# Kernel tuning notes

Hardware: AMD Instinct MI355X
Metric: run time of the kernel (lower is better)

## Reference

```python
import jax, jax.numpy as jnp
import numpy as np

H = 12
DK = 64


def setup_inputs() -> dict:
    key = jax.random.key(0)
    ks = jax.random.split(key, 6)
    bs, ne, d = 32, 20, H * DK
    R = jax.random.normal(ks[0], (bs, ne, ne, d), dtype=jnp.float32)
    R_mas = jax.random.randint(ks[1], (bs, ne, ne, 1), 0, 2).astype(jnp.float32)
    WQ_w = jax.random.normal(ks[2], (DK, DK), dtype=jnp.float32) * (1.0 / np.sqrt(DK))
    WK_w = jax.random.normal(ks[3], (DK, DK), dtype=jnp.float32) * (1.0 / np.sqrt(DK))
    WV_w = jax.random.normal(ks[4], (DK, DK), dtype=jnp.float32) * (1.0 / np.sqrt(DK))
    zb = jnp.zeros((DK,), dtype=jnp.float32)
    return {"R": R, "R_mas": R_mas, "WQ_w": WQ_w, "WQ_b": zb, "WK_w": WK_w,
            "WK_b": zb, "WV_w": WV_w, "WV_b": zb}


def reference(R, R_mas, WQ_w, WQ_b, WK_w, WK_b, WV_w, WV_b):
    bs, ne, _, d = R.shape
    h, dk = H, DK
    n = ne * ne
    # (bs, h, ne, ne, dk)
    Rh = R.reshape(bs, ne, ne, h, dk).transpose(0, 3, 1, 2, 4)
    # per-head QKV linears (torch Linear: y = x @ W.T + b)
    Q = (Rh @ WQ_w.T + WQ_b).reshape(bs, h, n, dk)
    K = (Rh @ WK_w.T + WK_b).reshape(bs, h, n, dk)
    V = (Rh @ WV_w.T + WV_b).reshape(bs, h, n, dk)
    mas = R_mas.reshape(bs, 1, n)                      # (bs,1,n)
    att_mas = mas[:, :, :, None] * mas[:, :, None, :]  # (bs,1,n,n)
    alpha = jnp.einsum('bhqd,bhkd->bhqk', Q, K)        # (bs,h,n,n)
    alpha = alpha - (1.0 - att_mas) * 100000.0         # mask BEFORE scaling (faithful)
    alpha = jax.nn.softmax(alpha / jnp.sqrt(jnp.float32(dk)), axis=-1)
    R_Z = jnp.einsum('bhqk,bhkd->bhqd', alpha, V).reshape(bs, h, ne, ne, dk)
    R_Z = R_Z * R_mas.reshape(bs, 1, ne, ne, 1)
    # (bs, ne, ne, h*dk)
    return R_Z.transpose(0, 2, 3, 1, 4).reshape(bs, ne, ne, h * dk)
```

## Files before the change

kernel.cpp:

```cpp
#include <hip/hip_runtime.h>

typedef float    f32x4 __attribute__((ext_vector_type(4)));
typedef _Float16 f16x8 __attribute__((ext_vector_type(8)));
typedef _Float16 f16x4 __attribute__((ext_vector_type(4)));
typedef _Float16 f16x2 __attribute__((ext_vector_type(2)));
typedef __fp16   fp16x2_raw __attribute__((ext_vector_type(2)));

#define MFMA16 __builtin_amdgcn_mfma_f32_16x16x32_f16

__device__ __forceinline__ f16x2 pkrtz(float a, float b) {
    fp16x2_raw t = __builtin_amdgcn_cvt_pkrtz(a, b);
    union { fp16x2_raw r; f16x2 h; } u;
    u.r = t;
    return u.h;
}
#define PKRTZ pkrtz

#define NQ     400
#define DMODEL 768

#define SCL 0.18033688011112042f
#define PEN 18033.688011112043f
#define M0  8.0f


#define K_OFF    0
#define VT_OFF   51200
#define W_OFF    105472
#define PEN_OFF  130048
#define BIAS_OFF 131648
#define MKB_OFF  132416
#define SMEM_BYTES 132480

__device__ __forceinline__ f16x8 cvt8(const float* rp) {
    f32x4 u0 = *(const f32x4*)(rp);
    f32x4 u1 = *(const f32x4*)(rp + 4);
    union { f16x2 h2[4]; f16x8 v; } u;
    u.h2[0] = PKRTZ(u0[0], u0[1]);
    u.h2[1] = PKRTZ(u0[2], u0[3]);
    u.h2[2] = PKRTZ(u1[0], u1[1]);
    u.h2[3] = PKRTZ(u1[2], u1[3]);
    return u.v;
}

__device__ __forceinline__ void proj_v(char* smem, f16x8 af0, f16x8 af1,
                                       int t, int g, int q16, int csw) {
    #pragma unroll
    for (int cg = 0; cg < 4; ++cg) {
        const int col = cg * 16 + q16;
        const float bb = *(const float*)(smem + BIAS_OFF + (128 + col) * 4);
        f32x4 acc = {bb, bb, bb, bb};
        f16x8 wb0 = *(const f16x8*)(smem + W_OFF + 16384 + col * 128 + ((g * 16) ^ csw));
        f16x8 wb1 = *(const f16x8*)(smem + W_OFF + 16384 + col * 128 + ((64 + g * 16) ^ csw));
        acc = MFMA16(af0, wb0, acc, 0, 0, 0);
        acc = MFMA16(af1, wb1, acc, 0, 0, 0);
        union { f16x2 h2[2]; f16x4 v; } hv;
        hv.h2[0] = PKRTZ(acc[0], acc[1]);
        hv.h2[1] = PKRTZ(acc[2], acc[3]);
        *(f16x4*)(smem + VT_OFF + col * 848 + (t >> 1) * 64 + g * 16 + (t & 1) * 8) = hv.v;
    }
}

__device__ __forceinline__ void proj_k(char* smem, f16x8 af0, f16x8 af1,
                                       int kk, int g, int q16, int csw) {
    #pragma unroll
    for (int cg = 0; cg < 4; ++cg) {
        const int d0 = cg * 16 + 4 * g;
        f32x4 acc = *(const f32x4*)(smem + BIAS_OFF + (64 + d0) * 4);
        f16x8 wb0 = *(const f16x8*)(smem + W_OFF + 8192 + (cg * 16 + q16) * 128 + ((g * 16) ^ csw));
        f16x8 wb1 = *(const f16x8*)(smem + W_OFF + 8192 + (cg * 16 + q16) * 128 + ((64 + g * 16) ^ csw));
        acc = MFMA16(wb0, af0, acc, 0, 0, 0);
        acc = MFMA16(wb1, af1, acc, 0, 0, 0);
        union { f16x2 h2[2]; f16x4 v; } hv;
        hv.h2[0] = PKRTZ(acc[0], acc[1]);
        hv.h2[1] = PKRTZ(acc[2], acc[3]);
        const int pos2 = ((cg & 2) << 5) + g * 16 + (cg & 1) * 8;
        *(f16x4*)(smem + K_OFF + kk * 128 + (pos2 ^ csw)) = hv.v;
    }
}

__device__ __forceinline__ void proj_q(char* smem, f16x8 af0, f16x8 af1,
                                       int g, int q16, int csw, f16x8 (&qreg)[2]) {
    f32x4 qa[4];
    #pragma unroll
    for (int cg = 0; cg < 4; ++cg) {
        const int d0 = cg * 16 + 4 * g;
        f32x4 acc = *(const f32x4*)(smem + BIAS_OFF + d0 * 4);
        f16x8 wb0 = *(const f16x8*)(smem + W_OFF + (cg * 16 + q16) * 128 + ((g * 16) ^ csw));
        f16x8 wb1 = *(const f16x8*)(smem + W_OFF + (cg * 16 + q16) * 128 + ((64 + g * 16) ^ csw));
        acc = MFMA16(wb0, af0, acc, 0, 0, 0);
        acc = MFMA16(wb1, af1, acc, 0, 0, 0);
        qa[cg] = acc;
    }
    union { f16x2 h2[4]; f16x8 v; } u0, u1;
    u0.h2[0] = PKRTZ(qa[0][0], qa[0][1]);
    u0.h2[1] = PKRTZ(qa[0][2], qa[0][3]);
    u0.h2[2] = PKRTZ(qa[1][0], qa[1][1]);
    u0.h2[3] = PKRTZ(qa[1][2], qa[1][3]);
    u1.h2[0] = PKRTZ(qa[2][0], qa[2][1]);
    u1.h2[1] = PKRTZ(qa[2][2], qa[2][3]);
    u1.h2[2] = PKRTZ(qa[3][0], qa[3][1]);
    u1.h2[3] = PKRTZ(qa[3][2], qa[3][3]);
    qreg[0] = u0.v;
    qreg[1] = u1.v;
}

__global__ __launch_bounds__(1024, 4)
void attn_fused(const float* __restrict__ R, const float* __restrict__ Rmas,
                const float* __restrict__ Wq, const float* __restrict__ bq,
                const float* __restrict__ Wk, const float* __restrict__ bk,
                const float* __restrict__ Wv, const float* __restrict__ bv,
                float* __restrict__ out)
{
    extern __shared__ char smem[];
    const int tid  = threadIdx.x;
    const int lane = tid & 63;
    const int wv   = tid >> 6;
    const int g    = lane >> 4;
    const int q16  = lane & 15;
    const int csw  = (q16 & 7) << 4;

    const int blk  = blockIdx.x;
    const int b    = blk / 24;
    const int rem  = blk - b * 24;
    const int h    = rem >> 1;
    const int half = rem & 1;
    const int qlo   = half ? 13 : 0;
    const int ntile = half ? 12 : 13;

    {
        if (tid < 768) {
            const int m   = tid >> 8;
            const int idx = tid & 255;
            const int row = idx >> 2;
            const int c0  = (idx & 3) << 4;
            const float* Wm = (m == 0 ? Wq : (m == 1 ? Wk : Wv)) + row * 64 + c0;
            const int sw = (row & 7) << 4;
            #pragma unroll
            for (int k2 = 0; k2 < 2; ++k2) {
                f32x4 v0 = *(const f32x4*)(Wm + 8 * k2);
                f32x4 v1 = *(const f32x4*)(Wm + 8 * k2 + 4);
                union { f16x2 h2[4]; f16x8 v; } hv;
                hv.h2[0] = PKRTZ(v0[0], v0[1]);
                hv.h2[1] = PKRTZ(v0[2], v0[3]);
                hv.h2[2] = PKRTZ(v1[0], v1[1]);
                hv.h2[3] = PKRTZ(v1[2], v1[3]);
                *(f16x8*)(smem + W_OFF + m * 8192 + row * 128 + ((c0 * 2 + 16 * k2) ^ sw)) = hv.v;
            }
        } else if (tid < 960) {
            const int j = tid - 768;
            const float* bms[3] = {bq, bk, bv};
            *(float*)(smem + BIAS_OFF + j * 4) = bms[j >> 6][j & 63];
        }
        if (wv < 7) {
            const int i = (wv << 6) | lane;
            const float mval = (i < NQ) ? Rmas[b * NQ + i] : 0.0f;
            unsigned long long bb = __ballot(mval != 0.0f);
            if (lane == 0) {
                ((unsigned*)(smem + MKB_OFF))[2 * wv]     = (unsigned)bb;
                ((unsigned*)(smem + MKB_OFF))[2 * wv + 1] = (unsigned)(bb >> 32);
            }
        }
        if (tid < 256) {
            const int r = tid >> 2, c = tid & 3;
            *(f16x4*)(smem + VT_OFF + r * 848 + 768 + c * 16 + 8) = (f16x4){0, 0, 0, 0};
        }
    }
    __syncthreads();

    const float* Rbh = R + (size_t)b * NQ * DMODEL + h * 64;

    f16x8 qreg[2];
    if (wv < ntile) {
        const int t = qlo + wv;
        const float* rp = Rbh + (size_t)(t * 16 + q16) * DMODEL + g * 8;
        f16x8 af0 = cvt8(rp);
        f16x8 af1 = cvt8(rp + 32);
        proj_q(smem, af0, af1, g, q16, csw, qreg);
        proj_k(smem, af0, af1, t * 16 + q16, g, q16, csw);
        proj_v(smem, af0, af1, t, g, q16, csw);
    }
    {
        const int  t  = half ? (wv - 3) : (9 + wv);
        const bool ok = half ? (wv >= 3) : (wv >= 4);
        if (ok) {
            const float* rp = Rbh + (size_t)(t * 16 + q16) * DMODEL + g * 8;
            f16x8 af0 = cvt8(rp);
            f16x8 af1 = cvt8(rp + 32);
            proj_k(smem, af0, af1, t * 16 + q16, g, q16, csw);
            proj_v(smem, af0, af1, t, g, q16, csw);
        }
    }
    if (wv == 0) {
        #pragma unroll
        for (int i = 0; i < 7; ++i) {
            const int k = i * 64 + lane;
            if (k < NQ) {
                const unsigned bit =
                    (((const unsigned*)(smem + MKB_OFF))[k >> 5] >> (k & 31)) & 1u;
                *(float*)(smem + PEN_OFF + k * 4) = bit ? -M0 : -(M0 + PEN);
            }
        }
    }
    __syncthreads();

    if (wv < ntile) {
        const int qt   = qlo + wv;
        const int qrow = qt * 16 + q16;
        const unsigned qb = (((const unsigned*)(smem + MKB_OFF))[qrow >> 5] >> (qrow & 31)) & 1u;

        const int kbase = K_OFF + q16 * 128;
        const int o0 = (g * 16) ^ csw;
        const int o1 = (64 + g * 16) ^ csw;

        f32x4 oc[4];
        #pragma unroll
        for (int cg = 0; cg < 4; ++cg) oc[cg] = (f32x4){0.f, 0.f, 0.f, 0.f};
        float ps = 0.f;

        f16x8 ka0 = *(const f16x8*)(smem + kbase + o0);
        f16x8 ka1 = *(const f16x8*)(smem + kbase + o1);
        f16x8 kb0 = *(const f16x8*)(smem + kbase + 2048 + o0);
        f16x8 kb1 = *(const f16x8*)(smem + kbase + 2048 + o1);

        #pragma unroll 1
        for (int kc = 0; kc < 12; ++kc) {
            f32x4 pa4 = *(const f32x4*)(smem + PEN_OFF + (kc * 32 + 4 * g) * 4);
            f32x4 pb4 = *(const f32x4*)(smem + PEN_OFF + (kc * 32 + 16 + 4 * g) * 4);

            f32x4 accA = {0.f, 0.f, 0.f, 0.f};
            accA = MFMA16(ka0, qreg[0], accA, 0, 0, 0);
            accA = MFMA16(ka1, qreg[1], accA, 0, 0, 0);
            f32x4 accB = {0.f, 0.f, 0.f, 0.f};
            accB = MFMA16(kb0, qreg[0], accB, 0, 0, 0);
            accB = MFMA16(kb1, qreg[1], accB, 0, 0, 0);

            const char* kn = smem + kbase + (kc + 1) * 4096;
            ka0 = *(const f16x8*)(kn + o0);
            ka1 = *(const f16x8*)(kn + o1);
            kb0 = *(const f16x8*)(kn + 2048 + o0);
            kb1 = *(const f16x8*)(kn + 2048 + o1);

            const float e0 = __builtin_amdgcn_exp2f(fmaf(accA[0], SCL, pa4[0]));
            const float e1 = __builtin_amdgcn_exp2f(fmaf(accA[1], SCL, pa4[1]));
            const float e2 = __builtin_amdgcn_exp2f(fmaf(accA[2], SCL, pa4[2]));
            const float e3 = __builtin_amdgcn_exp2f(fmaf(accA[3], SCL, pa4[3]));
            const float e4 = __builtin_amdgcn_exp2f(fmaf(accB[0], SCL, pb4[0]));
            const float e5 = __builtin_amdgcn_exp2f(fmaf(accB[1], SCL, pb4[1]));
            const float e6 = __builtin_amdgcn_exp2f(fmaf(accB[2], SCL, pb4[2]));
            const float e7 = __builtin_amdgcn_exp2f(fmaf(accB[3], SCL, pb4[3]));
            ps += ((e0 + e1) + (e2 + e3)) + ((e4 + e5) + (e6 + e7));

            union { f16x2 h2[4]; f16x8 v; } pu;
            pu.h2[0] = PKRTZ(e0, e1);
            pu.h2[1] = PKRTZ(e2, e3);
            pu.h2[2] = PKRTZ(e4, e5);
            pu.h2[3] = PKRTZ(e6, e7);
            const f16x8 pa = pu.v;
            #pragma unroll
            for (int cg = 0; cg < 4; ++cg) {
                f16x8 vb = *(const f16x8*)(smem + VT_OFF + (cg * 16 + q16) * 848 + kc * 64 + g * 16);
                oc[cg] = MFMA16(pa, vb, oc[cg], 0, 0, 0);
            }
        }
        {
            f32x4 pa4 = *(const f32x4*)(smem + PEN_OFF + (384 + 4 * g) * 4);
            f32x4 accA = {0.f, 0.f, 0.f, 0.f};
            accA = MFMA16(ka0, qreg[0], accA, 0, 0, 0);
            accA = MFMA16(ka1, qreg[1], accA, 0, 0, 0);
            const float e0 = __builtin_amdgcn_exp2f(fmaf(accA[0], SCL, pa4[0]));
            const float e1 = __builtin_amdgcn_exp2f(fmaf(accA[1], SCL, pa4[1]));
            const float e2 = __builtin_amdgcn_exp2f(fmaf(accA[2], SCL, pa4[2]));
            const float e3 = __builtin_amdgcn_exp2f(fmaf(accA[3], SCL, pa4[3]));
            ps += (e0 + e1) + (e2 + e3);
            union { f16x2 h2[4]; f16x8 v; } pu;
            pu.h2[0] = PKRTZ(e0, e1);
            pu.h2[1] = PKRTZ(e2, e3);
            pu.h2[2] = (f16x2){0, 0};
            pu.h2[3] = (f16x2){0, 0};
            const f16x8 pa = pu.v;
            #pragma unroll
            for (int cg = 0; cg < 4; ++cg) {
                f16x8 vb = *(const f16x8*)(smem + VT_OFF + (cg * 16 + q16) * 848 + 12 * 64 + g * 16);
                oc[cg] = MFMA16(pa, vb, oc[cg], 0, 0, 0);
            }
        }

        ps += __shfl_xor(ps, 16);
        ps += __shfl_xor(ps, 32);
        const float myrs = qb ? __builtin_amdgcn_rcpf(ps) : 0.0f;

        float rs[4];
        #pragma unroll
        for (int r = 0; r < 4; ++r) rs[r] = __shfl(myrs, 4 * g + r);
        float* op = out + (size_t)(b * NQ + qt * 16) * DMODEL + h * 64;
        #pragma unroll
        for (int r = 0; r < 4; ++r) {
            #pragma unroll
            for (int cg = 0; cg < 4; ++cg)
                op[(4 * g + r) * DMODEL + cg * 16 + q16] = oc[cg][r] * rs[r];
        }
    }
}

extern "C" void kernel_launch(void* const* d_in, const int* in_sizes, int n_in,
                              void* d_out, int out_size, void* d_ws, size_t ws_size,
                              hipStream_t stream) {
    const float* R    = (const float*)d_in[0];
    const float* Rmas = (const float*)d_in[1];
    const float* Wq   = (const float*)d_in[2];
    const float* bq   = (const float*)d_in[3];
    const float* Wk   = (const float*)d_in[4];
    const float* bk   = (const float*)d_in[5];
    const float* Wv   = (const float*)d_in[6];
    const float* bv   = (const float*)d_in[7];
    float* out = (float*)d_out;

    (void)hipFuncSetAttribute(reinterpret_cast<const void*>(attn_fused),
                              hipFuncAttributeMaxDynamicSharedMemorySize, SMEM_BYTES);
    attn_fused<<<dim3(768), dim3(1024), SMEM_BYTES, stream>>>(R, Rmas, Wq, bq, Wk, bk, Wv, bv, out);
}
```

Baseline: 47.97 us.

## Halve block size and have each wave process two query tiles

The kernel now launches 512-thread blocks (8 waves) instead of 1024. Each wave projects K/V for up to four key tiles and keeps Q for up to two query tiles, reusing each K fragment and V load across both query tiles in the attention loop. The weight-staging prologue is reorganised to fit the smaller block. The aim is to cut redundant LDS traffic and per-wave overhead, at the cost of fewer resident waves and an uneven split where some waves carry two tiles and others one.

```diff
diff --git a/kernel.cpp b/kernel.cpp
--- a/kernel.cpp
+++ b/kernel.cpp
@@ -22,7 +22,6 @@
 #define SCL 0.18033688011112042f
 #define PEN 18033.688011112043f
 #define M0  8.0f
-
 
 #define K_OFF    0
 #define VT_OFF   51200
@@ -105,7 +104,7 @@
     qreg[1] = u1.v;
 }
 
-__global__ __launch_bounds__(1024, 4)
+__global__ __launch_bounds__(512, 2)
 void attn_fused(const float* __restrict__ R, const float* __restrict__ Rmas,
                 const float* __restrict__ Wq, const float* __restrict__ bq,
                 const float* __restrict__ Wk, const float* __restrict__ bk,
@@ -125,32 +124,28 @@
     const int rem  = blk - b * 24;
     const int h    = rem >> 1;
     const int half = rem & 1;
-    const int qlo   = half ? 13 : 0;
-    const int ntile = half ? 12 : 13;
+    const int qlo  = half ? 13 : 0;
+    const int qhi  = half ? 25 : 13;
 
     {
-        if (tid < 768) {
-            const int m   = tid >> 8;
-            const int idx = tid & 255;
-            const int row = idx >> 2;
-            const int c0  = (idx & 3) << 4;
+        const int row = tid >> 3;
+        const int c0  = (tid & 7) << 3;
+        const int sw  = (row & 7) << 4;
+        #pragma unroll
+        for (int m = 0; m < 3; ++m) {
             const float* Wm = (m == 0 ? Wq : (m == 1 ? Wk : Wv)) + row * 64 + c0;
-            const int sw = (row & 7) << 4;
-            #pragma unroll
-            for (int k2 = 0; k2 < 2; ++k2) {
-                f32x4 v0 = *(const f32x4*)(Wm + 8 * k2);
-                f32x4 v1 = *(const f32x4*)(Wm + 8 * k2 + 4);
-                union { f16x2 h2[4]; f16x8 v; } hv;
-                hv.h2[0] = PKRTZ(v0[0], v0[1]);
-                hv.h2[1] = PKRTZ(v0[2], v0[3]);
-                hv.h2[2] = PKRTZ(v1[0], v1[1]);
-                hv.h2[3] = PKRTZ(v1[2], v1[3]);
-                *(f16x8*)(smem + W_OFF + m * 8192 + row * 128 + ((c0 * 2 + 16 * k2) ^ sw)) = hv.v;
-            }
-        } else if (tid < 960) {
-            const int j = tid - 768;
+            f32x4 v0 = *(const f32x4*)(Wm);
+            f32x4 v1 = *(const f32x4*)(Wm + 4);
+            union { f16x2 h2[4]; f16x8 v; } hv;
+            hv.h2[0] = PKRTZ(v0[0], v0[1]);
+            hv.h2[1] = PKRTZ(v0[2], v0[3]);
+            hv.h2[2] = PKRTZ(v1[0], v1[1]);
+            hv.h2[3] = PKRTZ(v1[2], v1[3]);
+            *(f16x8*)(smem + W_OFF + m * 8192 + row * 128 + ((c0 * 2) ^ sw)) = hv.v;
+        }
+        if (tid < 192) {
             const float* bms[3] = {bq, bk, bv};
-            *(float*)(smem + BIAS_OFF + j * 4) = bms[j >> 6][j & 63];
+            *(float*)(smem + BIAS_OFF + tid * 4) = bms[tid >> 6][tid & 63];
         }
         if (wv < 7) {
             const int i = (wv << 6) | lane;
@@ -170,25 +165,21 @@
 
     const float* Rbh = R + (size_t)b * NQ * DMODEL + h * 64;
 
-    f16x8 qreg[2];
-    if (wv < ntile) {
-        const int t = qlo + wv;
-        const float* rp = Rbh + (size_t)(t * 16 + q16) * DMODEL + g * 8;
-        f16x8 af0 = cvt8(rp);
-        f16x8 af1 = cvt8(rp + 32);
-        proj_q(smem, af0, af1, g, q16, csw, qreg);
-        proj_k(smem, af0, af1, t * 16 + q16, g, q16, csw);
-        proj_v(smem, af0, af1, t, g, q16, csw);
-    }
-    {
-        const int  t  = half ? (wv - 3) : (9 + wv);
-        const bool ok = half ? (wv >= 3) : (wv >= 4);
-        if (ok) {
+    f16x8 qreg0[2], qreg1[2];
+    int qt0 = -1, qt1 = -1;
+    #pragma unroll
+    for (int i = 0; i < 4; ++i) {
+        const int t = wv + 8 * i;
+        if (t < 25) {
             const float* rp = Rbh + (size_t)(t * 16 + q16) * DMODEL + g * 8;
             f16x8 af0 = cvt8(rp);
             f16x8 af1 = cvt8(rp + 32);
             proj_k(smem, af0, af1, t * 16 + q16, g, q16, csw);
             proj_v(smem, af0, af1, t, g, q16, csw);
+            if (t >= qlo && t < qhi) {
+                if (qt0 < 0) { proj_q(smem, af0, af1, g, q16, csw, qreg0); qt0 = t; }
+                else         { proj_q(smem, af0, af1, g, q16, csw, qreg1); qt1 = t; }
+            }
         }
     }
     if (wv == 0) {
@@ -204,19 +195,24 @@
     }
     __syncthreads();
 
-    if (wv < ntile) {
-        const int qt   = qlo + wv;
-        const int qrow = qt * 16 + q16;
-        const unsigned qb = (((const unsigned*)(smem + MKB_OFF))[qrow >> 5] >> (qrow & 31)) & 1u;
+    {
+        const bool has2 = (qt1 >= 0);
+        const int qrow0 = qt0 * 16 + q16;
+        const unsigned qb0 = (((const unsigned*)(smem + MKB_OFF))[qrow0 >> 5] >> (qrow0 & 31)) & 1u;
+        const int qrow1 = (has2 ? qt1 : qt0) * 16 + q16;
+        const unsigned qb1 = (((const unsigned*)(smem + MKB_OFF))[qrow1 >> 5] >> (qrow1 & 31)) & 1u;
 
         const int kbase = K_OFF + q16 * 128;
         const int o0 = (g * 16) ^ csw;
         const int o1 = (64 + g * 16) ^ csw;
 
-        f32x4 oc[4];
-        #pragma unroll
-        for (int cg = 0; cg < 4; ++cg) oc[cg] = (f32x4){0.f, 0.f, 0.f, 0.f};
-        float ps = 0.f;
+        f32x4 oc0[4], oc1[4];
+        #pragma unroll
+        for (int cg = 0; cg < 4; ++cg) {
+            oc0[cg] = (f32x4){0.f, 0.f, 0.f, 0.f};
+            oc1[cg] = (f32x4){0.f, 0.f, 0.f, 0.f};
+        }
+        float ps0 = 0.f, ps1 = 0.f;
 
         f16x8 ka0 = *(const f16x8*)(smem + kbase + o0);
         f16x8 ka1 = *(const f16x8*)(smem + kbase + o1);
@@ -228,12 +224,20 @@
             f32x4 pa4 = *(const f32x4*)(smem + PEN_OFF + (kc * 32 + 4 * g) * 4);
             f32x4 pb4 = *(const f32x4*)(smem + PEN_OFF + (kc * 32 + 16 + 4 * g) * 4);
 
-            f32x4 accA = {0.f, 0.f, 0.f, 0.f};
-            accA = MFMA16(ka0, qreg[0], accA, 0, 0, 0);
-            accA = MFMA16(ka1, qreg[1], accA, 0, 0, 0);
-            f32x4 accB = {0.f, 0.f, 0.f, 0.f};
-            accB = MFMA16(kb0, qreg[0], accB, 0, 0, 0);
-            accB = MFMA16(kb1, qreg[1], accB, 0, 0, 0);
+            f32x4 accA0 = {0.f, 0.f, 0.f, 0.f};
+            accA0 = MFMA16(ka0, qreg0[0], accA0, 0, 0, 0);
+            accA0 = MFMA16(ka1, qreg0[1], accA0, 0, 0, 0);
+            f32x4 accB0 = {0.f, 0.f, 0.f, 0.f};
+            accB0 = MFMA16(kb0, qreg0[0], accB0, 0, 0, 0);
+            accB0 = MFMA16(kb1, qreg0[1], accB0, 0, 0, 0);
+            f32x4 accA1 = {0.f, 0.f, 0.f, 0.f};
+            f32x4 accB1 = {0.f, 0.f, 0.f, 0.f};
+            if (has2) {
+                accA1 = MFMA16(ka0, qreg1[0], accA1, 0, 0, 0);
+                accA1 = MFMA16(ka1, qreg1[1], accA1, 0, 0, 0);
+                accB1 = MFMA16(kb0, qreg1[0], accB1, 0, 0, 0);
+                accB1 = MFMA16(kb1, qreg1[1], accB1, 0, 0, 0);
+            }
 
             const char* kn = smem + kbase + (kc + 1) * 4096;
             ka0 = *(const f16x8*)(kn + o0);
@@ -241,64 +245,116 @@
             kb0 = *(const f16x8*)(kn + 2048 + o0);
             kb1 = *(const f16x8*)(kn + 2048 + o1);
 
-            const float e0 = __builtin_amdgcn_exp2f(fmaf(accA[0], SCL, pa4[0]));
-            const float e1 = __builtin_amdgcn_exp2f(fmaf(accA[1], SCL, pa4[1]));
-            const float e2 = __builtin_amdgcn_exp2f(fmaf(accA[2], SCL, pa4[2]));
-            const float e3 = __builtin_amdgcn_exp2f(fmaf(accA[3], SCL, pa4[3]));
-            const float e4 = __builtin_amdgcn_exp2f(fmaf(accB[0], SCL, pb4[0]));
-            const float e5 = __builtin_amdgcn_exp2f(fmaf(accB[1], SCL, pb4[1]));
-            const float e6 = __builtin_amdgcn_exp2f(fmaf(accB[2], SCL, pb4[2]));
-            const float e7 = __builtin_amdgcn_exp2f(fmaf(accB[3], SCL, pb4[3]));
-            ps += ((e0 + e1) + (e2 + e3)) + ((e4 + e5) + (e6 + e7));
-
-            union { f16x2 h2[4]; f16x8 v; } pu;
-            pu.h2[0] = PKRTZ(e0, e1);
-            pu.h2[1] = PKRTZ(e2, e3);
-            pu.h2[2] = PKRTZ(e4, e5);
-            pu.h2[3] = PKRTZ(e6, e7);
-            const f16x8 pa = pu.v;
+            const float e0 = __builtin_amdgcn_exp2f(fmaf(accA0[0], SCL, pa4[0]));
+            const float e1 = __builtin_amdgcn_exp2f(fmaf(accA0[1], SCL, pa4[1]));
+            const float e2 = __builtin_amdgcn_exp2f(fmaf(accA0[2], SCL, pa4[2]));
+            const float e3 = __builtin_amdgcn_exp2f(fmaf(accA0[3], SCL, pa4[3]));
+            const float e4 = __builtin_amdgcn_exp2f(fmaf(accB0[0], SCL, pb4[0]));
+            const float e5 = __builtin_amdgcn_exp2f(fmaf(accB0[1], SCL, pb4[1]));
+            const float e6 = __builtin_amdgcn_exp2f(fmaf(accB0[2], SCL, pb4[2]));
+            const float e7 = __builtin_amdgcn_exp2f(fmaf(accB0[3], SCL, pb4[3]));
+            ps0 += ((e0 + e1) + (e2 + e3)) + ((e4 + e5) + (e6 + e7));
+            union { f16x2 h2[4]; f16x8 v; } pu0;
+            pu0.h2[0] = PKRTZ(e0, e1);
+            pu0.h2[1] = PKRTZ(e2, e3);
+            pu0.h2[2] = PKRTZ(e4, e5);
+            pu0.h2[3] = PKRTZ(e6, e7);
+            const f16x8 pfrag0 = pu0.v;
+
+            f16x8 pfrag1;
+            if (has2) {
+                const float f0 = __builtin_amdgcn_exp2f(fmaf(accA1[0], SCL, pa4[0]));
+                const float f1 = __builtin_amdgcn_exp2f(fmaf(accA1[1], SCL, pa4[1]));
+                const float f2 = __builtin_amdgcn_exp2f(fmaf(accA1[2], SCL, pa4[2]));
+                const float f3 = __builtin_amdgcn_exp2f(fmaf(accA1[3], SCL, pa4[3]));
+                const float f4 = __builtin_amdgcn_exp2f(fmaf(accB1[0], SCL, pb4[0]));
+                const float f5 = __builtin_amdgcn_exp2f(fmaf(accB1[1], SCL, pb4[1]));
+                const float f6 = __builtin_amdgcn_exp2f(fmaf(accB1[2], SCL, pb4[2]));
+                const float f7 = __builtin_amdgcn_exp2f(fmaf(accB1[3], SCL, pb4[3]));
+                ps1 += ((f0 + f1) + (f2 + f3)) + ((f4 + f5) + (f6 + f7));
+                union { f16x2 h2[4]; f16x8 v; } pu1;
+                pu1.h2[0] = PKRTZ(f0, f1);
+                pu1.h2[1] = PKRTZ(f2, f3);
+                pu1.h2[2] = PKRTZ(f4, f5);
+                pu1.h2[3] = PKRTZ(f6, f7);
+                pfrag1 = pu1.v;
+            }
+
             #pragma unroll
             for (int cg = 0; cg < 4; ++cg) {
                 f16x8 vb = *(const f16x8*)(smem + VT_OFF + (cg * 16 + q16) * 848 + kc * 64 + g * 16);
-                oc[cg] = MFMA16(pa, vb, oc[cg], 0, 0, 0);
+                oc0[cg] = MFMA16(pfrag0, vb, oc0[cg], 0, 0, 0);
+                if (has2) oc1[cg] = MFMA16(pfrag1, vb, oc1[cg], 0, 0, 0);
             }
         }
         {
             f32x4 pa4 = *(const f32x4*)(smem + PEN_OFF + (384 + 4 * g) * 4);
-            f32x4 accA = {0.f, 0.f, 0.f, 0.f};
-            accA = MFMA16(ka0, qreg[0], accA, 0, 0, 0);
-            accA = MFMA16(ka1, qreg[1], accA, 0, 0, 0);
-            const float e0 = __builtin_amdgcn_exp2f(fmaf(accA[0], SCL, pa4[0]));
-            const float e1 = __builtin_amdgcn_exp2f(fmaf(accA[1], SCL, pa4[1]));
-            const float e2 = __builtin_amdgcn_exp2f(fmaf(accA[2], SCL, pa4[2]));
-            const float e3 = __builtin_amdgcn_exp2f(fmaf(accA[3], SCL, pa4[3]));
-            ps += (e0 + e1) + (e2 + e3);
-            union { f16x2 h2[4]; f16x8 v; } pu;
-            pu.h2[0] = PKRTZ(e0, e1);
-            pu.h2[1] = PKRTZ(e2, e3);
-            pu.h2[2] = (f16x2){0, 0};
-            pu.h2[3] = (f16x2){0, 0};
-            const f16x8 pa = pu.v;
+            f32x4 accA0 = {0.f, 0.f, 0.f, 0.f};
+            accA0 = MFMA16(ka0, qreg0[0], accA0, 0, 0, 0);
+            accA0 = MFMA16(ka1, qreg0[1], accA0, 0, 0, 0);
+            const float e0 = __builtin_amdgcn_exp2f(fmaf(accA0[0], SCL, pa4[0]));
+            const float e1 = __builtin_amdgcn_exp2f(fmaf(accA0[1], SCL, pa4[1]));
+            const float e2 = __builtin_amdgcn_exp2f(fmaf(accA0[2], SCL, pa4[2]));
+            const float e3 = __builtin_amdgcn_exp2f(fmaf(accA0[3], SCL, pa4[3]));
+            ps0 += (e0 + e1) + (e2 + e3);
+            union { f16x2 h2[4]; f16x8 v; } pu0;
+            pu0.h2[0] = PKRTZ(e0, e1);
+            pu0.h2[1] = PKRTZ(e2, e3);
+            pu0.h2[2] = (f16x2){0, 0};
+            pu0.h2[3] = (f16x2){0, 0};
+            const f16x8 pfrag0 = pu0.v;
+
+            f16x8 pfrag1;
+            if (has2) {
+                f32x4 accA1 = {0.f, 0.f, 0.f, 0.f};
+                accA1 = MFMA16(ka0, qreg1[0], accA1, 0, 0, 0);
+                accA1 = MFMA16(ka1, qreg1[1], accA1, 0, 0, 0);
+                const float f0 = __builtin_amdgcn_exp2f(fmaf(accA1[0], SCL, pa4[0]));
+                const float f1 = __builtin_amdgcn_exp2f(fmaf(accA1[1], SCL, pa4[1]));
+                const float f2 = __builtin_amdgcn_exp2f(fmaf(accA1[2], SCL, pa4[2]));
+                const float f3 = __builtin_amdgcn_exp2f(fmaf(accA1[3], SCL, pa4[3]));
+                ps1 += (f0 + f1) + (f2 + f3);
+                union { f16x2 h2[4]; f16x8 v; } pu1;
+                pu1.h2[0] = PKRTZ(f0, f1);
+                pu1.h2[1] = PKRTZ(f2, f3);
+                pu1.h2[2] = (f16x2){0, 0};
+                pu1.h2[3] = (f16x2){0, 0};
+                pfrag1 = pu1.v;
+            }
             #pragma unroll
             for (int cg = 0; cg < 4; ++cg) {
                 f16x8 vb = *(const f16x8*)(smem + VT_OFF + (cg * 16 + q16) * 848 + 12 * 64 + g * 16);
-                oc[cg] = MFMA16(pa, vb, oc[cg], 0, 0, 0);
-            }
-        }
-
-        ps += __shfl_xor(ps, 16);
-        ps += __shfl_xor(ps, 32);
-        const float myrs = qb ? __builtin_amdgcn_rcpf(ps) : 0.0f;
-
+                oc0[cg] = MFMA16(pfrag0, vb, oc0[cg], 0, 0, 0);
+                if (has2) oc1[cg] = MFMA16(pfrag1, vb, oc1[cg], 0, 0, 0);
+            }
+        }
+
+        ps0 += __shfl_xor(ps0, 16);
+        ps0 += __shfl_xor(ps0, 32);
+        const float myrs0 = qb0 ? __builtin_amdgcn_rcpf(ps0) : 0.0f;
         float rs[4];
         #pragma unroll
-        for (int r = 0; r < 4; ++r) rs[r] = __shfl(myrs, 4 * g + r);
-        float* op = out + (size_t)(b * NQ + qt * 16) * DMODEL + h * 64;
+        for (int r = 0; r < 4; ++r) rs[r] = __shfl(myrs0, 4 * g + r);
+        float* op0 = out + (size_t)(b * NQ + qt0 * 16) * DMODEL + h * 64;
         #pragma unroll
         for (int r = 0; r < 4; ++r) {
             #pragma unroll
             for (int cg = 0; cg < 4; ++cg)
-                op[(4 * g + r) * DMODEL + cg * 16 + q16] = oc[cg][r] * rs[r];
+                op0[(4 * g + r) * DMODEL + cg * 16 + q16] = oc0[cg][r] * rs[r];
+        }
+        if (has2) {
+            ps1 += __shfl_xor(ps1, 16);
+            ps1 += __shfl_xor(ps1, 32);
+            const float myrs1 = qb1 ? __builtin_amdgcn_rcpf(ps1) : 0.0f;
+            #pragma unroll
+            for (int r = 0; r < 4; ++r) rs[r] = __shfl(myrs1, 4 * g + r);
+            float* op1 = out + (size_t)(b * NQ + qt1 * 16) * DMODEL + h * 64;
+            #pragma unroll
+            for (int r = 0; r < 4; ++r) {
+                #pragma unroll
+                for (int cg = 0; cg < 4; ++cg)
+                    op1[(4 * g + r) * DMODEL + cg * 16 + q16] = oc1[cg][r] * rs[r];
+            }
         }
     }
 }
@@ -318,5 +374,5 @@
 
     (void)hipFuncSetAttribute(reinterpret_cast<const void*>(attn_fused),
                               hipFuncAttributeMaxDynamicSharedMemorySize, SMEM_BYTES);
-    attn_fused<<<dim3(768), dim3(1024), SMEM_BYTES, stream>>>(R, Rmas, Wq, bq, Wk, bk, Wv, bv, out);
-}
+    attn_fused<<<dim3(768), dim3(512), SMEM_BYTES, stream>>>(R, Rmas, Wq, bq, Wk, bk, Wv, bv, out);
+}
```

Result: slower. 51.50 us (+7.4%).
